# Kernel optimization log

Measured on AMD Instinct MI355X. Metric: run time of the kernel, lower is better.

The kernel has to match this reference:

```python
import jax, jax.numpy as jnp
import numpy as np

N = 100000
E_RAND = 800000
IN_D, HID_D, OUT_D = 128, 64, 64
PROP_STEP = 8
ATTN_AFT = PROP_STEP // 2  # attention applied after this many prop steps
LAM = 1.0
ALP = 1.0 / (LAM + 1.0)    # alp=0 in init -> DGL auto-sets 1/(lam+1)
TAU = 0.2
P_RHO = 1.0
T_UP = -1.0                # T<=0 -> no upper threshold


def setup_inputs() -> dict:
    key = jax.random.key(0)
    k1, k2, k3, k4, k5 = jax.random.split(key, 5)
    loops = jnp.arange(N)
    src = jnp.concatenate([jax.random.randint(k1, (E_RAND,), 0, N), loops]).astype(jnp.int32)
    dst = jnp.concatenate([jax.random.randint(k2, (E_RAND,), 0, N), loops]).astype(jnp.int32)
    feat = jax.random.normal(k3, (N, IN_D), jnp.float32)
    # xavier_normal init, zero bias (as in MLP.reset_params)
    W_bef = jax.random.normal(k4, (IN_D, HID_D), jnp.float32) * np.float32(np.sqrt(2.0 / (IN_D + HID_D)))
    b_bef = jnp.zeros((HID_D,), jnp.float32)
    W_aft = jax.random.normal(k5, (HID_D, OUT_D), jnp.float32) * np.float32(np.sqrt(2.0 / (HID_D + OUT_D)))
    b_aft = jnp.zeros((OUT_D,), jnp.float32)
    return {"feat": feat, "W_bef": W_bef, "b_bef": b_bef, "W_aft": W_aft, "b_aft": b_aft, "src": src, "dst": dst}


def _ax(src, dst, w, X):
    # Y = A X with per-edge weights: scatter-add of w_e * X[src_e] into dst_e
    return jax.ops.segment_sum(X[src] * w[:, None], dst, num_segments=N)


def _attention(src, dst, Y):
    hs, hd = Y[src], Y[dst]  # [E, d]
    w = jnp.sum(hs * hs, -1) + jnp.sum(hd * hd, -1) - 2.0 * jnp.sum(hs * hd, -1)  # ||h_u - h_v||^2
    w = jax.nn.relu(w) + 1e-7
    w = jnp.power(w, 1.0 - 0.5 * P_RHO)
    w = jnp.maximum(w, TAU)  # lower threshold tau (in-place clamp in torch)
    if T_UP > 0:
        w = jnp.where(w > T_UP, jnp.inf, w)
    w = 1.0 / w + 1e-9
    deg = jax.ops.segment_sum(w, dst, num_segments=N)  # copy_e -> sum per dst node
    return w, deg


def _prop(src, dst, w, deg, Y, X):
    dt = LAM * deg + (1.0 - LAM)
    nrm = jnp.power(dt, -0.5)[:, None]
    py = nrm * _ax(src, dst, w, nrm * Y)
    return (1.0 - ALP) * Y + ALP * LAM * py + ALP * (X / dt[:, None])


def reference(feat, W_bef, b_bef, W_aft, b_aft, src, dst):
    X = feat @ W_bef + b_bef  # mlp_bef: single Linear(input_d, hidden_d)
    w = jnp.ones(src.shape[0], feat.dtype)  # initial edge weights = 1
    deg = jax.ops.segment_sum(w, dst, num_segments=N)  # in-degrees
    Y = X
    for k in range(PROP_STEP):
        Y = _prop(src, dst, w, deg, Y, X)
        if k == ATTN_AFT - 1:
            w, deg = _attention(src, dst, Y)
    # mlp_aft: init_activate=True (relu; norm='none', dropout=0) then Linear(hidden_d, output_d)
    return jax.nn.relu(Y) @ W_aft + b_aft
```

## Files before the change

### kernel.cpp

```cpp
#include <hip/hip_runtime.h>
#include <math.h>

#define IN_D 128
#define HID 64


__global__ void zero_ints(int* a, int n) {
    int i = blockIdx.x * blockDim.x + threadIdx.x;
    if (i < n) a[i] = 0;
}

__global__ void hist_kernel(const int* __restrict__ dst, int E, int* __restrict__ cnt) {
    int e = blockIdx.x * blockDim.x + threadIdx.x;
    if (e < E) atomicAdd(&cnt[dst[e]], 1);
}

__global__ void scan1_kernel(const int* __restrict__ cnt, int N,
                             int* __restrict__ row_ptr, int* __restrict__ blocksum) {
    __shared__ int sm[1024];
    int i = blockIdx.x * 1024 + threadIdx.x;
    int v = (i < N) ? cnt[i] : 0;
    sm[threadIdx.x] = v;
    __syncthreads();
    for (int off = 1; off < 1024; off <<= 1) {
        int t = (threadIdx.x >= off) ? sm[threadIdx.x - off] : 0;
        __syncthreads();
        sm[threadIdx.x] += t;
        __syncthreads();
    }
    if (i < N) row_ptr[i + 1] = sm[threadIdx.x];
    if (threadIdx.x == 1023) blocksum[blockIdx.x] = sm[1023];
}

__global__ void scan2_kernel(int* __restrict__ blocksum, int nb) {
    __shared__ int sm[1024];
    int v = (threadIdx.x < nb) ? blocksum[threadIdx.x] : 0;
    sm[threadIdx.x] = v;
    __syncthreads();
    for (int off = 1; off < 1024; off <<= 1) {
        int t = (threadIdx.x >= off) ? sm[threadIdx.x - off] : 0;
        __syncthreads();
        sm[threadIdx.x] += t;
        __syncthreads();
    }
    if (threadIdx.x < nb) blocksum[threadIdx.x] = sm[threadIdx.x] - v;
}

__global__ void scan3_kernel(int* __restrict__ row_ptr, int N, const int* __restrict__ blocksum) {
    int i = blockIdx.x * 1024 + threadIdx.x;
    if (i < N) row_ptr[i + 1] += blocksum[blockIdx.x];
    if (i == 0) row_ptr[0] = 0;
}

__global__ void scatter_kernel(const int* __restrict__ src, const int* __restrict__ dst, int E,
                               const int* __restrict__ row_ptr, int* __restrict__ cursor,
                               int* __restrict__ src_perm) {
    int e = blockIdx.x * blockDim.x + threadIdx.x;
    if (e < E) {
        int d = dst[e];
        int pos = row_ptr[d] + atomicAdd(&cursor[d], 1);
        src_perm[pos] = src[e];
    }
}

__global__ void degnrm_from_cnt(const int* __restrict__ cnt, int N,
                                float* __restrict__ nrm, float* __restrict__ invdt) {
    int i = blockIdx.x * blockDim.x + threadIdx.x;
    if (i < N) {
        float d = (float)cnt[i];
        nrm[i] = 1.0f / sqrtf(d);
        invdt[i] = 1.0f / d;
    }
}

__global__ void nrm_from_deg(const float* __restrict__ deg, int N,
                             float* __restrict__ nrm, float* __restrict__ invdt) {
    int i = blockIdx.x * blockDim.x + threadIdx.x;
    if (i < N) {
        float dt = deg[i];
        nrm[i] = 1.0f / sqrtf(dt);
        invdt[i] = 1.0f / dt;
    }
}

__global__ void coef_kernel(const int* __restrict__ src_perm, const float* __restrict__ w_perm,
                            const float* __restrict__ nrm, int E, float* __restrict__ coef) {
    int e = blockIdx.x * blockDim.x + threadIdx.x;
    if (e < E) {
        float c = nrm[src_perm[e]];
        if (w_perm) c *= w_perm[e];
        coef[e] = c;
    }
}


__global__ __launch_bounds__(256) void prop_kernel(
    const float* __restrict__ Yin, const float* __restrict__ X,
    const int* __restrict__ row_ptr, const int* __restrict__ src_perm,
    const float* __restrict__ coef, const float* __restrict__ nrm,
    const float* __restrict__ invdt, int N, float* __restrict__ Yout) {
    int wave = (blockIdx.x * blockDim.x + threadIdx.x) >> 6;
    int lane = threadIdx.x & 63;
    if (wave >= N) return;
    int r0 = row_ptr[wave], r1 = row_ptr[wave + 1];
    float acc = 0.0f;
    for (int jb = r0; jb < r1; jb += 64) {
        int m = r1 - jb;
        if (m > 64) m = 64;
        int sv = 0;
        float cv = 0.0f;
        if (lane < m) { sv = src_perm[jb + lane]; cv = coef[jb + lane]; }
        for (int t = 0; t < m; t += 8) {
            float v[8], c[8];
            #pragma unroll
            for (int u = 0; u < 8; ++u) {
                int idx = t + u;
                int active = idx < m;
                if (!active) idx = 0;
                int s = __shfl(sv, idx, 64);
                float cc = __shfl(cv, idx, 64);
                c[u] = active ? cc : 0.0f;
                v[u] = Yin[(size_t)s * HID + lane];
            }
            #pragma unroll
            for (int u = 0; u < 8; ++u) acc += c[u] * v[u];
        }
    }
    size_t base = (size_t)wave * HID + lane;
    Yout[base] = 0.5f * Yin[base] + (0.5f * nrm[wave]) * acc + (0.5f * invdt[wave]) * X[base];
}

__global__ __launch_bounds__(256) void attn_kernel(
    const float* __restrict__ Y, const int* __restrict__ row_ptr,
    const int* __restrict__ src_perm, int N,
    float* __restrict__ w_perm, float* __restrict__ deg) {
    int wv = (blockIdx.x * blockDim.x + threadIdx.x) >> 6;
    int lane = threadIdx.x & 63;
    if (wv >= N) return;
    int r0 = row_ptr[wv], r1 = row_ptr[wv + 1];
    float hd = Y[(size_t)wv * HID + lane];
    float dacc = 0.0f;
    for (int jb = r0; jb < r1; jb += 64) {
        int m = r1 - jb;
        if (m > 64) m = 64;
        int sv = (lane < m) ? src_perm[jb + lane] : 0;
        float wreg = 0.0f;
        for (int t = 0; t < m; t += 4) {
            float ss[4];
            int act[4];
            #pragma unroll
            for (int u = 0; u < 4; ++u) {
                int idx = t + u;
                act[u] = idx < m;
                if (!act[u]) idx = 0;
                int s = __shfl(sv, idx, 64);
                float d = Y[(size_t)s * HID + lane] - hd;
                ss[u] = d * d;
            }
            #pragma unroll
            for (int o = 32; o >= 1; o >>= 1) {
                #pragma unroll
                for (int u = 0; u < 4; ++u) ss[u] += __shfl_xor(ss[u], o, 64);
            }
            #pragma unroll
            for (int u = 0; u < 4; ++u) {
                float w = fmaxf(ss[u], 0.0f) + 1e-7f;
                w = sqrtf(w);
                w = fmaxf(w, 0.2f);
                w = 1.0f / w + 1e-9f;
                if (act[u]) {
                    dacc += w;
                    if (lane == t + u) wreg = w;
                }
            }
        }
        if (lane < m) w_perm[jb + lane] = wreg;
    }
    if (lane == 0) deg[wv] = dacc;
}

__global__ __launch_bounds__(256) void gemm1_kernel(
    const float* __restrict__ feat, const float* __restrict__ W,
    const float* __restrict__ b, int N, float* __restrict__ X) {
    __shared__ float Wl[IN_D * HID];
    __shared__ float featL[8 * IN_D];
    for (int i = threadIdx.x; i < IN_D * HID; i += 256) Wl[i] = W[i];
    int c = threadIdx.x & 63;
    int rsub = threadIdx.x >> 6;
    float bias = b[c];
    int ngroups = N / 8;
    const float4* feat4 = (const float4*)feat;
    for (int g = blockIdx.x; g < ngroups; g += gridDim.x) {
        __syncthreads();
        ((float4*)featL)[threadIdx.x] = feat4[(size_t)g * 256 + threadIdx.x];
        __syncthreads();
        const float4* f0 = (const float4*)&featL[rsub * IN_D];
        const float4* f1 = (const float4*)&featL[(rsub + 4) * IN_D];
        float acc0 = bias, acc1 = bias;
        #pragma unroll
        for (int k4 = 0; k4 < IN_D / 4; ++k4) {
            float4 a = f0[k4];
            float4 e = f1[k4];
            float w0 = Wl[(4 * k4 + 0) * HID + c];
            float w1 = Wl[(4 * k4 + 1) * HID + c];
            float w2 = Wl[(4 * k4 + 2) * HID + c];
            float w3 = Wl[(4 * k4 + 3) * HID + c];
            acc0 += a.x * w0 + a.y * w1 + a.z * w2 + a.w * w3;
            acc1 += e.x * w0 + e.y * w1 + e.z * w2 + e.w * w3;
        }
        size_t row = (size_t)g * 8;
        X[(row + rsub) * HID + c] = acc0;
        X[(row + rsub + 4) * HID + c] = acc1;
    }
}

__global__ __launch_bounds__(256) void gemm2_kernel(
    const float* __restrict__ Y, const float* __restrict__ W,
    const float* __restrict__ b, int N, float* __restrict__ out) {
    __shared__ float Wl[HID * HID];
    __shared__ float Yl[8 * HID];
    for (int i = threadIdx.x; i < HID * HID; i += 256) Wl[i] = W[i];
    int c = threadIdx.x & 63;
    int rsub = threadIdx.x >> 6;
    float bias = b[c];
    int ngroups = N / 8;
    const float4* Y4 = (const float4*)Y;
    for (int g = blockIdx.x; g < ngroups; g += gridDim.x) {
        __syncthreads();
        if (threadIdx.x < 128) {
            float4 v = Y4[(size_t)g * 128 + threadIdx.x];
            v.x = fmaxf(v.x, 0.0f); v.y = fmaxf(v.y, 0.0f);
            v.z = fmaxf(v.z, 0.0f); v.w = fmaxf(v.w, 0.0f);
            ((float4*)Yl)[threadIdx.x] = v;
        }
        __syncthreads();
        const float4* f0 = (const float4*)&Yl[rsub * HID];
        const float4* f1 = (const float4*)&Yl[(rsub + 4) * HID];
        float acc0 = bias, acc1 = bias;
        #pragma unroll
        for (int k4 = 0; k4 < HID / 4; ++k4) {
            float4 a = f0[k4];
            float4 e = f1[k4];
            float w0 = Wl[(4 * k4 + 0) * HID + c];
            float w1 = Wl[(4 * k4 + 1) * HID + c];
            float w2 = Wl[(4 * k4 + 2) * HID + c];
            float w3 = Wl[(4 * k4 + 3) * HID + c];
            acc0 += a.x * w0 + a.y * w1 + a.z * w2 + a.w * w3;
            acc1 += e.x * w0 + e.y * w1 + e.z * w2 + e.w * w3;
        }
        size_t row = (size_t)g * 8;
        out[(row + rsub) * HID + c] = acc0;
        out[(row + rsub + 4) * HID + c] = acc1;
    }
}


extern "C" void kernel_launch(void* const* d_in, const int* in_sizes, int n_in,
                              void* d_out, int out_size, void* d_ws, size_t ws_size,
                              hipStream_t stream) {
    const float* feat  = (const float*)d_in[0];
    const float* W_bef = (const float*)d_in[1];
    const float* b_bef = (const float*)d_in[2];
    const float* W_aft = (const float*)d_in[3];
    const float* b_aft = (const float*)d_in[4];
    const int*   src   = (const int*)d_in[5];
    const int*   dst   = (const int*)d_in[6];

    const int N = in_sizes[0] / IN_D;
    const int E = in_sizes[5];

    char* p = (char*)d_ws;
    auto alloc = [&](size_t bytes) -> void* {
        void* r = (void*)p;
        p += (bytes + 255) & ~(size_t)255;
        return r;
    };
    float* X       = (float*)alloc((size_t)N * HID * 4);
    float* Ya      = (float*)alloc((size_t)N * HID * 4);
    float* Yb      = (float*)alloc((size_t)N * HID * 4);
    int*   cnt     = (int*)alloc((size_t)N * 4);
    int*   cursor  = (int*)alloc((size_t)N * 4);
    int*   row_ptr = (int*)alloc((size_t)(N + 1) * 4);
    int*   blocksum= (int*)alloc(4096);
    int*   src_perm= (int*)alloc((size_t)E * 4);
    float* w_perm  = (float*)alloc((size_t)E * 4);
    float* coef    = (float*)alloc((size_t)E * 4);
    float* deg     = (float*)alloc((size_t)N * 4);
    float* nrm     = (float*)alloc((size_t)N * 4);
    float* invdt   = (float*)alloc((size_t)N * 4);

    const int TB = 256;
    dim3 blk(TB);
    int gN   = (N + TB - 1) / TB;
    int gE   = (E + TB - 1) / TB;
    int gNW  = (N * 64 + TB - 1) / TB;
    int nb   = (N + 1023) / 1024;

    zero_ints<<<gN, blk, 0, stream>>>(cnt, N);
    zero_ints<<<gN, blk, 0, stream>>>(cursor, N);
    hist_kernel<<<gE, blk, 0, stream>>>(dst, E, cnt);
    scan1_kernel<<<nb, 1024, 0, stream>>>(cnt, N, row_ptr, blocksum);
    scan2_kernel<<<1, 1024, 0, stream>>>(blocksum, nb);
    scan3_kernel<<<nb, 1024, 0, stream>>>(row_ptr, N, blocksum);
    degnrm_from_cnt<<<gN, blk, 0, stream>>>(cnt, N, nrm, invdt);
    scatter_kernel<<<gE, blk, 0, stream>>>(src, dst, E, row_ptr, cursor, src_perm);

    gemm1_kernel<<<2048, blk, 0, stream>>>(feat, W_bef, b_bef, N, X);

    coef_kernel<<<gE, blk, 0, stream>>>(src_perm, nullptr, nrm, E, coef);
    prop_kernel<<<gNW, blk, 0, stream>>>(X,  X, row_ptr, src_perm, coef, nrm, invdt, N, Ya);
    prop_kernel<<<gNW, blk, 0, stream>>>(Ya, X, row_ptr, src_perm, coef, nrm, invdt, N, Yb);
    prop_kernel<<<gNW, blk, 0, stream>>>(Yb, X, row_ptr, src_perm, coef, nrm, invdt, N, Ya);
    prop_kernel<<<gNW, blk, 0, stream>>>(Ya, X, row_ptr, src_perm, coef, nrm, invdt, N, Yb);

    attn_kernel<<<gNW, blk, 0, stream>>>(Yb, row_ptr, src_perm, N, w_perm, deg);
    nrm_from_deg<<<gN, blk, 0, stream>>>(deg, N, nrm, invdt);
    coef_kernel<<<gE, blk, 0, stream>>>(src_perm, w_perm, nrm, E, coef);

    prop_kernel<<<gNW, blk, 0, stream>>>(Yb, X, row_ptr, src_perm, coef, nrm, invdt, N, Ya);
    prop_kernel<<<gNW, blk, 0, stream>>>(Ya, X, row_ptr, src_perm, coef, nrm, invdt, N, Yb);
    prop_kernel<<<gNW, blk, 0, stream>>>(Yb, X, row_ptr, src_perm, coef, nrm, invdt, N, Ya);
    prop_kernel<<<gNW, blk, 0, stream>>>(Ya, X, row_ptr, src_perm, coef, nrm, invdt, N, Yb);

    gemm2_kernel<<<512, blk, 0, stream>>>(Yb, W_aft, b_aft, N, (float*)d_out);
}
```

Measured before the change: 714.5 us.

## Gather neighbor features from bf16 shadow copies and fuse setup kernels

Each propagation step now writes a bf16 copy of Y next to the fp32 output. The neighbor gathers in the prop and attention kernels read that bf16 copy, which halves the bytes pulled by the random-access gather. The degree/norm computation is folded into scan1, the initial coef computation into the scatter kernel, and the two zeroing kernels are merged, which removes several launches. The attention inner loop is unrolled by 8 instead of 4. This adds extra bf16 writes per step and rounds the aggregated neighbor values to bf16, which costs some accuracy.

```diff
diff --git a/kernel.cpp b/kernel.cpp
--- a/kernel.cpp
+++ b/kernel.cpp
@@ -4,10 +4,22 @@
 #define IN_D 128
 #define HID 64
 
-
-__global__ void zero_ints(int* a, int n) {
+typedef unsigned short ushort_t;
+typedef unsigned int uint_t;
+
+static __device__ __forceinline__ ushort_t f2bf(float f) {
+    uint_t x = __float_as_uint(f);
+    uint_t r = x + 0x7fffu + ((x >> 16) & 1u);
+    return (ushort_t)(r >> 16);
+}
+static __device__ __forceinline__ float bf2f(ushort_t u) {
+    return __uint_as_float(((uint_t)u) << 16);
+}
+
+
+__global__ void zero2_kernel(int* a, int* b, int n) {
     int i = blockIdx.x * blockDim.x + threadIdx.x;
-    if (i < n) a[i] = 0;
+    if (i < n) { a[i] = 0; b[i] = 0; }
 }
 
 __global__ void hist_kernel(const int* __restrict__ dst, int E, int* __restrict__ cnt) {
@@ -16,10 +28,16 @@
 }
 
 __global__ void scan1_kernel(const int* __restrict__ cnt, int N,
-                             int* __restrict__ row_ptr, int* __restrict__ blocksum) {
+                             int* __restrict__ row_ptr, int* __restrict__ blocksum,
+                             float* __restrict__ nrm, float* __restrict__ invdt) {
     __shared__ int sm[1024];
     int i = blockIdx.x * 1024 + threadIdx.x;
     int v = (i < N) ? cnt[i] : 0;
+    if (i < N) {
+        float d = (float)v;
+        nrm[i] = 1.0f / sqrtf(d);
+        invdt[i] = 1.0f / d;
+    }
     sm[threadIdx.x] = v;
     __syncthreads();
     for (int off = 1; off < 1024; off <<= 1) {
@@ -54,22 +72,15 @@
 
 __global__ void scatter_kernel(const int* __restrict__ src, const int* __restrict__ dst, int E,
                                const int* __restrict__ row_ptr, int* __restrict__ cursor,
-                               int* __restrict__ src_perm) {
+                               const float* __restrict__ nrm,
+                               int* __restrict__ src_perm, float* __restrict__ coef) {
     int e = blockIdx.x * blockDim.x + threadIdx.x;
     if (e < E) {
         int d = dst[e];
+        int s = src[e];
         int pos = row_ptr[d] + atomicAdd(&cursor[d], 1);
-        src_perm[pos] = src[e];
-    }
-}
-
-__global__ void degnrm_from_cnt(const int* __restrict__ cnt, int N,
-                                float* __restrict__ nrm, float* __restrict__ invdt) {
-    int i = blockIdx.x * blockDim.x + threadIdx.x;
-    if (i < N) {
-        float d = (float)cnt[i];
-        nrm[i] = 1.0f / sqrtf(d);
-        invdt[i] = 1.0f / d;
+        src_perm[pos] = s;
+        coef[pos] = nrm[s];
     }
 }
 
@@ -86,19 +97,17 @@
 __global__ void coef_kernel(const int* __restrict__ src_perm, const float* __restrict__ w_perm,
                             const float* __restrict__ nrm, int E, float* __restrict__ coef) {
     int e = blockIdx.x * blockDim.x + threadIdx.x;
-    if (e < E) {
-        float c = nrm[src_perm[e]];
-        if (w_perm) c *= w_perm[e];
-        coef[e] = c;
-    }
+    if (e < E) coef[e] = w_perm[e] * nrm[src_perm[e]];
 }
 
 
 __global__ __launch_bounds__(256) void prop_kernel(
-    const float* __restrict__ Yin, const float* __restrict__ X,
+    const float* __restrict__ Yin, const ushort_t* __restrict__ Ybf,
+    const float* __restrict__ X,
     const int* __restrict__ row_ptr, const int* __restrict__ src_perm,
     const float* __restrict__ coef, const float* __restrict__ nrm,
-    const float* __restrict__ invdt, int N, float* __restrict__ Yout) {
+    const float* __restrict__ invdt, int N,
+    float* __restrict__ Yout, ushort_t* __restrict__ Yout_bf) {
     int wave = (blockIdx.x * blockDim.x + threadIdx.x) >> 6;
     int lane = threadIdx.x & 63;
     if (wave >= N) return;
@@ -120,19 +129,21 @@
                 int s = __shfl(sv, idx, 64);
                 float cc = __shfl(cv, idx, 64);
                 c[u] = active ? cc : 0.0f;
-                v[u] = Yin[(size_t)s * HID + lane];
+                v[u] = bf2f(Ybf[(size_t)s * HID + lane]);
             }
             #pragma unroll
             for (int u = 0; u < 8; ++u) acc += c[u] * v[u];
         }
     }
     size_t base = (size_t)wave * HID + lane;
-    Yout[base] = 0.5f * Yin[base] + (0.5f * nrm[wave]) * acc + (0.5f * invdt[wave]) * X[base];
+    float out = 0.5f * Yin[base] + (0.5f * nrm[wave]) * acc + (0.5f * invdt[wave]) * X[base];
+    Yout[base] = out;
+    Yout_bf[base] = f2bf(out);
 }
 
 __global__ __launch_bounds__(256) void attn_kernel(
-    const float* __restrict__ Y, const int* __restrict__ row_ptr,
-    const int* __restrict__ src_perm, int N,
+    const float* __restrict__ Y, const ushort_t* __restrict__ Ybf,
+    const int* __restrict__ row_ptr, const int* __restrict__ src_perm, int N,
     float* __restrict__ w_perm, float* __restrict__ deg) {
     int wv = (blockIdx.x * blockDim.x + threadIdx.x) >> 6;
     int lane = threadIdx.x & 63;
@@ -145,25 +156,25 @@
         if (m > 64) m = 64;
         int sv = (lane < m) ? src_perm[jb + lane] : 0;
         float wreg = 0.0f;
-        for (int t = 0; t < m; t += 4) {
-            float ss[4];
-            int act[4];
-            #pragma unroll
-            for (int u = 0; u < 4; ++u) {
+        for (int t = 0; t < m; t += 8) {
+            float ss[8];
+            int act[8];
+            #pragma unroll
+            for (int u = 0; u < 8; ++u) {
                 int idx = t + u;
                 act[u] = idx < m;
                 if (!act[u]) idx = 0;
                 int s = __shfl(sv, idx, 64);
-                float d = Y[(size_t)s * HID + lane] - hd;
+                float d = bf2f(Ybf[(size_t)s * HID + lane]) - hd;
                 ss[u] = d * d;
             }
             #pragma unroll
             for (int o = 32; o >= 1; o >>= 1) {
                 #pragma unroll
-                for (int u = 0; u < 4; ++u) ss[u] += __shfl_xor(ss[u], o, 64);
+                for (int u = 0; u < 8; ++u) ss[u] += __shfl_xor(ss[u], o, 64);
             }
             #pragma unroll
-            for (int u = 0; u < 4; ++u) {
+            for (int u = 0; u < 8; ++u) {
                 float w = fmaxf(ss[u], 0.0f) + 1e-7f;
                 w = sqrtf(w);
                 w = fmaxf(w, 0.2f);
@@ -181,7 +192,7 @@
 
 __global__ __launch_bounds__(256) void gemm1_kernel(
     const float* __restrict__ feat, const float* __restrict__ W,
-    const float* __restrict__ b, int N, float* __restrict__ X) {
+    const float* __restrict__ b, int N, float* __restrict__ X, ushort_t* __restrict__ Xbf) {
     __shared__ float Wl[IN_D * HID];
     __shared__ float featL[8 * IN_D];
     for (int i = threadIdx.x; i < IN_D * HID; i += 256) Wl[i] = W[i];
@@ -211,6 +222,8 @@
         size_t row = (size_t)g * 8;
         X[(row + rsub) * HID + c] = acc0;
         X[(row + rsub + 4) * HID + c] = acc1;
+        Xbf[(row + rsub) * HID + c] = f2bf(acc0);
+        Xbf[(row + rsub + 4) * HID + c] = f2bf(acc1);
     }
 }
 
@@ -275,19 +288,22 @@
         p += (bytes + 255) & ~(size_t)255;
         return r;
     };
-    float* X       = (float*)alloc((size_t)N * HID * 4);
-    float* Ya      = (float*)alloc((size_t)N * HID * 4);
-    float* Yb      = (float*)alloc((size_t)N * HID * 4);
-    int*   cnt     = (int*)alloc((size_t)N * 4);
-    int*   cursor  = (int*)alloc((size_t)N * 4);
-    int*   row_ptr = (int*)alloc((size_t)(N + 1) * 4);
-    int*   blocksum= (int*)alloc(4096);
-    int*   src_perm= (int*)alloc((size_t)E * 4);
-    float* w_perm  = (float*)alloc((size_t)E * 4);
-    float* coef    = (float*)alloc((size_t)E * 4);
-    float* deg     = (float*)alloc((size_t)N * 4);
-    float* nrm     = (float*)alloc((size_t)N * 4);
-    float* invdt   = (float*)alloc((size_t)N * 4);
+    float*    X       = (float*)alloc((size_t)N * HID * 4);
+    float*    Ya      = (float*)alloc((size_t)N * HID * 4);
+    float*    Yb      = (float*)alloc((size_t)N * HID * 4);
+    ushort_t* Xbf     = (ushort_t*)alloc((size_t)N * HID * 2);
+    ushort_t* Yabf    = (ushort_t*)alloc((size_t)N * HID * 2);
+    ushort_t* Ybbf    = (ushort_t*)alloc((size_t)N * HID * 2);
+    int*      cnt     = (int*)alloc((size_t)N * 4);
+    int*      cursor  = (int*)alloc((size_t)N * 4);
+    int*      row_ptr = (int*)alloc((size_t)(N + 1) * 4);
+    int*      blocksum= (int*)alloc(4096);
+    int*      src_perm= (int*)alloc((size_t)E * 4);
+    float*    w_perm  = (float*)alloc((size_t)E * 4);
+    float*    coef    = (float*)alloc((size_t)E * 4);
+    float*    deg     = (float*)alloc((size_t)N * 4);
+    float*    nrm     = (float*)alloc((size_t)N * 4);
+    float*    invdt   = (float*)alloc((size_t)N * 4);
 
     const int TB = 256;
     dim3 blk(TB);
@@ -296,31 +312,28 @@
     int gNW  = (N * 64 + TB - 1) / TB;
     int nb   = (N + 1023) / 1024;
 
-    zero_ints<<<gN, blk, 0, stream>>>(cnt, N);
-    zero_ints<<<gN, blk, 0, stream>>>(cursor, N);
+    zero2_kernel<<<gN, blk, 0, stream>>>(cnt, cursor, N);
     hist_kernel<<<gE, blk, 0, stream>>>(dst, E, cnt);
-    scan1_kernel<<<nb, 1024, 0, stream>>>(cnt, N, row_ptr, blocksum);
+    scan1_kernel<<<nb, 1024, 0, stream>>>(cnt, N, row_ptr, blocksum, nrm, invdt);
     scan2_kernel<<<1, 1024, 0, stream>>>(blocksum, nb);
     scan3_kernel<<<nb, 1024, 0, stream>>>(row_ptr, N, blocksum);
-    degnrm_from_cnt<<<gN, blk, 0, stream>>>(cnt, N, nrm, invdt);
-    scatter_kernel<<<gE, blk, 0, stream>>>(src, dst, E, row_ptr, cursor, src_perm);
-
-    gemm1_kernel<<<2048, blk, 0, stream>>>(feat, W_bef, b_bef, N, X);
-
-    coef_kernel<<<gE, blk, 0, stream>>>(src_perm, nullptr, nrm, E, coef);
-    prop_kernel<<<gNW, blk, 0, stream>>>(X,  X, row_ptr, src_perm, coef, nrm, invdt, N, Ya);
-    prop_kernel<<<gNW, blk, 0, stream>>>(Ya, X, row_ptr, src_perm, coef, nrm, invdt, N, Yb);
-    prop_kernel<<<gNW, blk, 0, stream>>>(Yb, X, row_ptr, src_perm, coef, nrm, invdt, N, Ya);
-    prop_kernel<<<gNW, blk, 0, stream>>>(Ya, X, row_ptr, src_perm, coef, nrm, invdt, N, Yb);
-
-    attn_kernel<<<gNW, blk, 0, stream>>>(Yb, row_ptr, src_perm, N, w_perm, deg);
+    scatter_kernel<<<gE, blk, 0, stream>>>(src, dst, E, row_ptr, cursor, nrm, src_perm, coef);
+
+    gemm1_kernel<<<2048, blk, 0, stream>>>(feat, W_bef, b_bef, N, X, Xbf);
+
+    prop_kernel<<<gNW, blk, 0, stream>>>(X,  Xbf,  X, row_ptr, src_perm, coef, nrm, invdt, N, Ya, Yabf);
+    prop_kernel<<<gNW, blk, 0, stream>>>(Ya, Yabf, X, row_ptr, src_perm, coef, nrm, invdt, N, Yb, Ybbf);
+    prop_kernel<<<gNW, blk, 0, stream>>>(Yb, Ybbf, X, row_ptr, src_perm, coef, nrm, invdt, N, Ya, Yabf);
+    prop_kernel<<<gNW, blk, 0, stream>>>(Ya, Yabf, X, row_ptr, src_perm, coef, nrm, invdt, N, Yb, Ybbf);
+
+    attn_kernel<<<gNW, blk, 0, stream>>>(Yb, Ybbf, row_ptr, src_perm, N, w_perm, deg);
     nrm_from_deg<<<gN, blk, 0, stream>>>(deg, N, nrm, invdt);
     coef_kernel<<<gE, blk, 0, stream>>>(src_perm, w_perm, nrm, E, coef);
 
-    prop_kernel<<<gNW, blk, 0, stream>>>(Yb, X, row_ptr, src_perm, coef, nrm, invdt, N, Ya);
-    prop_kernel<<<gNW, blk, 0, stream>>>(Ya, X, row_ptr, src_perm, coef, nrm, invdt, N, Yb);
-    prop_kernel<<<gNW, blk, 0, stream>>>(Yb, X, row_ptr, src_perm, coef, nrm, invdt, N, Ya);
-    prop_kernel<<<gNW, blk, 0, stream>>>(Ya, X, row_ptr, src_perm, coef, nrm, invdt, N, Yb);
+    prop_kernel<<<gNW, blk, 0, stream>>>(Yb, Ybbf, X, row_ptr, src_perm, coef, nrm, invdt, N, Ya, Yabf);
+    prop_kernel<<<gNW, blk, 0, stream>>>(Ya, Yabf, X, row_ptr, src_perm, coef, nrm, invdt, N, Yb, Ybbf);
+    prop_kernel<<<gNW, blk, 0, stream>>>(Yb, Ybbf, X, row_ptr, src_perm, coef, nrm, invdt, N, Ya, Yabf);
+    prop_kernel<<<gNW, blk, 0, stream>>>(Ya, Yabf, X, row_ptr, src_perm, coef, nrm, invdt, N, Yb, Ybbf);
 
     gemm2_kernel<<<512, blk, 0, stream>>>(Yb, W_aft, b_aft, N, (float*)d_out);
 }
```

Measured after the change: 719.5 us. About the same (+0.7%).
